# Optimization experiments

Hardware: AMD Instinct MI355X
Metric: run time of the kernel (lower is better)

## Reference

```python
import math
import jax, jax.numpy as jnp
import numpy as np

B, S, HID = 2, 1024, 1024
NH, HD = 16, 64
WIN = 4096
CACHE = 3072
EPS = 1e-5


def _clinear(xr, xi, Wr, Wi, br, bi):
    # complex linear: (xr + i xi)(Wr + i Wi)^T + (br + i bi)
    yr = xr @ Wr.T - xi @ Wi.T + br
    yi = xr @ Wi.T + xi @ Wr.T + bi
    return yr, yi


def _forward(hidden_re, hidden_im, K_cache_re, K_cache_im, V_cache_re, V_cache_im,
             gamma, beta_re, beta_im,
             q_Wr, q_Wi, q_br, q_bi, k_Wr, k_Wi, k_br, k_bi,
             v_Wr, v_Wi, v_br, v_bi, o_Wr, o_Wi, o_br, o_bi):
    batch, seq, _ = hidden_re.shape
    # --- complex LayerNorm: center complex mean, normalize by sqrt(E|x-mu|^2) ---
    mur = hidden_re.mean(-1, keepdims=True)
    mui = hidden_im.mean(-1, keepdims=True)
    cr = hidden_re - mur
    ci = hidden_im - mui
    inv = jax.lax.rsqrt((cr * cr + ci * ci).mean(-1, keepdims=True) + EPS)
    nr = cr * inv * gamma + beta_re
    ni = ci * inv * gamma + beta_im
    # --- projections ---
    Qr, Qi = _clinear(nr, ni, q_Wr, q_Wi, q_br, q_bi)
    Kr, Ki = _clinear(nr, ni, k_Wr, k_Wi, k_br, k_bi)
    Vr, Vi = _clinear(nr, ni, v_Wr, v_Wi, v_br, v_bi)
    Qr = Qr.reshape(batch, seq, NH, HD)
    Qi = Qi.reshape(batch, seq, NH, HD)
    Kr = Kr.reshape(batch, seq, NH, HD)
    Ki = Ki.reshape(batch, seq, NH, HD)
    Vr = Vr.reshape(batch, seq, NH, HD)
    Vi = Vi.reshape(batch, seq, NH, HD)
    # --- KV cache concat + window eviction (static shapes) ---
    cache_len = K_cache_re.shape[1]
    Kr = jnp.concatenate([K_cache_re, Kr], axis=1)
    Ki = jnp.concatenate([K_cache_im, Ki], axis=1)
    Vr = jnp.concatenate([V_cache_re, Vr], axis=1)
    Vi = jnp.concatenate([V_cache_im, Vi], axis=1)
    total_kv = Kr.shape[1]
    if total_kv > WIN:
        drop = total_kv - WIN
        Kr, Ki, Vr, Vi = Kr[:, drop:], Ki[:, drop:], Vr[:, drop:], Vi[:, drop:]
        cache_len = max(0, cache_len - drop)
        total_kv = WIN
    # --- Hermitian scores: Re(Q K^H) = Qr.Kr + Qi.Ki ---
    scale = 1.0 / math.sqrt(HD)
    scores = (jnp.einsum('bshd,bthd->bhst', Qr, Kr)
              + jnp.einsum('bshd,bthd->bhst', Qi, Ki)) * scale
    rows = jnp.arange(seq)[:, None]
    cols = jnp.arange(total_kv)[None, :]
    allowed = cols <= rows + cache_len  # causal within current chunk, full cache visible
    scores = jnp.where(allowed, scores, jnp.float32(-1e30))
    weights = jax.nn.softmax(scores, axis=-1)  # [B,NH,S,T]
    outr = jnp.einsum('bhst,bthd->bshd', weights, Vr).reshape(batch, seq, NH * HD)
    outi = jnp.einsum('bhst,bthd->bshd', weights, Vi).reshape(batch, seq, NH * HD)
    dr, di = _clinear(outr, outi, o_Wr, o_Wi, o_br, o_bi)
    out_re = hidden_re + dr
    out_im = hidden_im + di
    new_K_re, new_K_im = Kr[:, -WIN:], Ki[:, -WIN:]
    new_V_re, new_V_im = Vr[:, -WIN:], Vi[:, -WIN:]
    return out_re, out_im, new_K_re, new_K_im, new_V_re, new_V_im


def setup_inputs() -> dict:
    key = jax.random.key(0)
    ks = jax.random.split(key, 16)
    w = 0.02
    d = {
        'hidden_re': jax.random.normal(ks[0], (B, S, HID), jnp.float32),
        'hidden_im': jax.random.normal(ks[1], (B, S, HID), jnp.float32),
        'K_cache_re': jax.random.normal(ks[2], (B, CACHE, NH, HD), jnp.float32),
        'K_cache_im': jax.random.normal(ks[3], (B, CACHE, NH, HD), jnp.float32),
        'V_cache_re': jax.random.normal(ks[4], (B, CACHE, NH, HD), jnp.float32),
        'V_cache_im': jax.random.normal(ks[5], (B, CACHE, NH, HD), jnp.float32),
        'gamma': jnp.ones((HID,), jnp.float32),
        'beta_re': jnp.zeros((HID,), jnp.float32),
        'beta_im': jnp.zeros((HID,), jnp.float32),
    }
    for i, p in enumerate(['q', 'k', 'v', 'o']):
        d[p + '_Wr'] = jax.random.normal(ks[6 + 2 * i], (HID, HID), jnp.float32) * w
        d[p + '_Wi'] = jax.random.normal(ks[7 + 2 * i], (HID, HID), jnp.float32) * w
        d[p + '_br'] = jnp.zeros((HID,), jnp.float32)
        d[p + '_bi'] = jnp.zeros((HID,), jnp.float32)
    return d


def reference(hidden_re, hidden_im, K_cache_re, K_cache_im, V_cache_re, V_cache_im,
              gamma, beta_re, beta_im,
              q_Wr, q_Wi, q_br, q_bi, k_Wr, k_Wi, k_br, k_bi,
              v_Wr, v_Wi, v_br, v_bi, o_Wr, o_Wi, o_br, o_bi):
    return _forward(hidden_re, hidden_im, K_cache_re, K_cache_im, V_cache_re, V_cache_im,
                    gamma, beta_re, beta_im,
                    q_Wr, q_Wi, q_br, q_bi, k_Wr, k_Wi, k_br, k_bi,
                    v_Wr, v_Wi, v_br, v_bi, o_Wr, o_Wi, o_br, o_bi)
```

## Files before the change

kernel.cpp:

```cpp
#include <hip/hip_runtime.h>
#include <hip/hip_bf16.h>
#include <cstdint>
#include <cstddef>

typedef __bf16 bf16x8 __attribute__((ext_vector_type(8)));
typedef float  f32x4  __attribute__((ext_vector_type(4)));

__device__ __forceinline__ unsigned short f2bf(float f) {
  union { float f; unsigned u; } v; v.f = f;
  unsigned u = v.u;
  u += 0x7FFFu + ((u >> 16) & 1u);
  return (unsigned short)(u >> 16);
}

__device__ __forceinline__ unsigned short f2bf_cvt(float f) {
  __bf16 h = (__bf16)f;
  return __builtin_bit_cast(unsigned short, h);
}

struct alignas(16) US8 { unsigned short u[8]; };

__device__ __forceinline__ void g2lds16(const void* g, void* l) {
  __builtin_amdgcn_global_load_lds(
      (const __attribute__((address_space(1))) unsigned int*)g,
      (__attribute__((address_space(3))) unsigned int*)l, 16, 0, 0);
}

#define BB 2
#define SS 1024
#define HID 1024
#define NHH 16
#define HDD 64
#define TT 4096
#define CCH 3072
#define QSCALE (0.125f * 1.44269504088896f)

__global__ __launch_bounds__(256) void ln_kernel(
    const float* __restrict__ hre, const float* __restrict__ him,
    const float* __restrict__ gamma, const float* __restrict__ bre,
    const float* __restrict__ bim, unsigned short* __restrict__ Aln)
{
  int m = blockIdx.x;
  int tid = threadIdx.x;
  const float4 vr = ((const float4*)(hre + (size_t)m * HID))[tid];
  const float4 vi = ((const float4*)(him + (size_t)m * HID))[tid];
  float sr = vr.x + vr.y + vr.z + vr.w;
  float si = vi.x + vi.y + vi.z + vi.w;
  float sq = vr.x*vr.x + vr.y*vr.y + vr.z*vr.z + vr.w*vr.w
           + vi.x*vi.x + vi.y*vi.y + vi.z*vi.z + vi.w*vi.w;
  __shared__ float red[3][4];
  int lane = tid & 63, w = tid >> 6;
  for (int off = 32; off; off >>= 1) {
    sr += __shfl_down(sr, off, 64);
    si += __shfl_down(si, off, 64);
    sq += __shfl_down(sq, off, 64);
  }
  if (lane == 0) { red[0][w] = sr; red[1][w] = si; red[2][w] = sq; }
  __syncthreads();
  sr = red[0][0] + red[0][1] + red[0][2] + red[0][3];
  si = red[1][0] + red[1][1] + red[1][2] + red[1][3];
  sq = red[2][0] + red[2][1] + red[2][2] + red[2][3];
  float mur = sr * (1.f/1024.f), mui = si * (1.f/1024.f);
  float var = sq * (1.f/1024.f) - mur*mur - mui*mui;
  float inv = rsqrtf(var + 1e-5f);
  int k = tid * 4;
  float4 g  = ((const float4*)gamma)[tid];
  float4 br = ((const float4*)bre)[tid];
  float4 bi = ((const float4*)bim)[tid];
  ushort4 nr, ni;
  nr.x = f2bf((vr.x - mur) * inv * g.x + br.x);
  nr.y = f2bf((vr.y - mur) * inv * g.y + br.y);
  nr.z = f2bf((vr.z - mur) * inv * g.z + br.z);
  nr.w = f2bf((vr.w - mur) * inv * g.w + br.w);
  ni.x = f2bf((vi.x - mui) * inv * g.x + bi.x);
  ni.y = f2bf((vi.y - mui) * inv * g.y + bi.y);
  ni.z = f2bf((vi.z - mui) * inv * g.z + bi.z);
  ni.w = f2bf((vi.w - mui) * inv * g.w + bi.w);
  *(ushort4*)&Aln[(size_t)m * 2048 + k]        = nr;
  *(ushort4*)&Aln[(size_t)m * 2048 + 1024 + k] = ni;
}

__global__ __launch_bounds__(256) void wprep_kernel(
    const float* __restrict__ qWr, const float* __restrict__ qWi,
    const float* __restrict__ kWr, const float* __restrict__ kWi,
    const float* __restrict__ vWr, const float* __restrict__ vWi,
    const float* __restrict__ oWr, const float* __restrict__ oWi,
    unsigned short* __restrict__ Wc)
{
  int gid = blockIdx.x * 256 + threadIdx.x;
  int idx = gid * 8;
  int p   = idx >> 22;
  int rem = idx & 0x3FFFFF;
  int n   = rem >> 11;
  int k   = rem & 2047;
  const float* Wr; const float* Wi;
  switch (p) {
    case 0:  Wr = qWr; Wi = qWi; break;
    case 1:  Wr = kWr; Wi = kWi; break;
    case 2:  Wr = vWr; Wi = vWi; break;
    default: Wr = oWr; Wi = oWi; break;
  }
  const float* src; float sgn = 1.f;
  if (n < 1024) {
    if (k < 1024) src = Wr + (size_t)n * 1024 + k;
    else        { src = Wi + (size_t)n * 1024 + (k - 1024); sgn = -1.f; }
  } else {
    if (k < 1024) src = Wi + (size_t)(n - 1024) * 1024 + k;
    else          src = Wr + (size_t)(n - 1024) * 1024 + (k - 1024);
  }
  float4 a = ((const float4*)src)[0];
  float4 b = ((const float4*)src)[1];
  US8 o;
  o.u[0] = f2bf(a.x * sgn); o.u[1] = f2bf(a.y * sgn);
  o.u[2] = f2bf(a.z * sgn); o.u[3] = f2bf(a.w * sgn);
  o.u[4] = f2bf(b.x * sgn); o.u[5] = f2bf(b.y * sgn);
  o.u[6] = f2bf(b.z * sgn); o.u[7] = f2bf(b.w * sgn);
  *(US8*)&Wc[idx] = o;
}

__global__ __launch_bounds__(256) void bprep_kernel(
    const float* __restrict__ qbr, const float* __restrict__ qbi,
    const float* __restrict__ kbr, const float* __restrict__ kbi,
    const float* __restrict__ vbr, const float* __restrict__ vbi,
    const float* __restrict__ obr, const float* __restrict__ obi,
    float* __restrict__ bc)
{
  int idx = blockIdx.x * 256 + threadIdx.x;
  int p = idx >> 11, n = idx & 2047;
  const float* br; const float* bi;
  switch (p) {
    case 0:  br = qbr; bi = qbi; break;
    case 1:  br = kbr; bi = kbi; break;
    case 2:  br = vbr; bi = vbi; break;
    default: br = obr; bi = obi; break;
  }
  bc[idx] = (n < 1024) ? br[n] : bi[n - 1024];
}

__global__ __launch_bounds__(256) void gemm_qkv_kernel(
    const unsigned short* __restrict__ A, const unsigned short* __restrict__ Bm,
    const float* __restrict__ bias,
    unsigned short* __restrict__ Qp, unsigned short* __restrict__ Kp,
    float* __restrict__ out_Kre, float* __restrict__ out_Kim,
    float* __restrict__ out_Vre, float* __restrict__ out_Vim)
{
  __shared__ alignas(16) unsigned short As[128][32];
  __shared__ alignas(16) unsigned short Bs[128][32];
  const int K = 2048;
  int bm = blockIdx.y * 128;
  int bn = blockIdx.x * 128;
  int tid = threadIdx.x;
  int lane = tid & 63, w = tid >> 6;
  int wm = (w >> 1) * 64, wn = (w & 1) * 64;
  int l15 = lane & 15, q = lane >> 4;
  int lr = tid >> 2;
  int lc = (tid & 3) * 8;

  f32x4 acc[4][4] = {};

  for (int k0 = 0; k0 < K; k0 += 32) {
    g2lds16(&A [(size_t)(bm + lr)      * K + k0 + lc], (unsigned short*)As + 8*tid);
    g2lds16(&A [(size_t)(bm + lr + 64) * K + k0 + lc], (unsigned short*)As + 2048 + 8*tid);
    g2lds16(&Bm[(size_t)(bn + lr)      * K + k0 + lc], (unsigned short*)Bs + 8*tid);
    g2lds16(&Bm[(size_t)(bn + lr + 64) * K + k0 + lc], (unsigned short*)Bs + 2048 + 8*tid);
    __syncthreads();
    bf16x8 af[4], bfr[4];
#pragma unroll
    for (int i = 0; i < 4; i++) af[i]  = *(const bf16x8*)&As[wm + i*16 + l15][q*8];
#pragma unroll
    for (int i = 0; i < 4; i++) bfr[i] = *(const bf16x8*)&Bs[wn + i*16 + l15][q*8];
#pragma unroll
    for (int i = 0; i < 4; i++)
#pragma unroll
      for (int j = 0; j < 4; j++)
        acc[i][j] = __builtin_amdgcn_mfma_f32_16x16x32_bf16(af[i], bfr[j], acc[i][j], 0, 0, 0);
    __syncthreads();
  }

  const int sec = bn >> 11;
#pragma unroll
  for (int i = 0; i < 4; i++)
#pragma unroll
    for (int j = 0; j < 4; j++) {
      int n = bn + wn + j*16 + l15;
      float bv = bias[n];
      int col = n & 2047;
      int re = (col < 1024) ? 1 : 0;
      int h = (col & 1023) >> 6, d = col & 63;
      int d2 = re ? d : 64 + d;
#pragma unroll
      for (int r = 0; r < 4; r++) {
        int m = bm + wm + i*16 + q*4 + r;
        float val = acc[i][j][r] + bv;
        int b = m >> 10, s = m & 1023;
        int bh = b*16 + h;
        if (sec == 0) {
          Qp[((size_t)bh*1024 + s)*128 + d2] = f2bf(val * QSCALE);
        } else if (sec == 1) {
          int t = CCH + s;
          Kp[((size_t)bh*4096 + t)*128 + d2] = f2bf(val);
          float* dst = re ? out_Kre : out_Kim;
          dst[(((size_t)b*4096 + t)*16 + h)*64 + d] = val;
        } else {
          int t = CCH + s;
          float* dst = re ? out_Vre : out_Vim;
          dst[(((size_t)b*4096 + t)*16 + h)*64 + d] = val;
        }
      }
    }
}

__global__ __launch_bounds__(256) void gemm_oproj_kernel(
    const unsigned short* __restrict__ A, const unsigned short* __restrict__ Bm,
    const float* __restrict__ bias, const float* __restrict__ hre,
    const float* __restrict__ him, float* __restrict__ out)
{
  __shared__ alignas(16) unsigned short As[128][32];
  __shared__ alignas(16) unsigned short Bs[128][32];
  int bm = blockIdx.y * 128;
  int bn = blockIdx.x * 128;
  int tid = threadIdx.x;
  int lane = tid & 63, w = tid >> 6;
  int wm = (w >> 1) * 64, wn = (w & 1) * 64;
  int l15 = lane & 15, q = lane >> 4;
  int lr = tid >> 2;
  int lc = (tid & 3) * 8;
  const int K = 2048;

  f32x4 acc[4][4] = {};

  for (int k0 = 0; k0 < K; k0 += 32) {
    g2lds16(&A [(size_t)(bm + lr)      * K + k0 + lc], (unsigned short*)As + 8*tid);
    g2lds16(&A [(size_t)(bm + lr + 64) * K + k0 + lc], (unsigned short*)As + 2048 + 8*tid);
    g2lds16(&Bm[(size_t)(bn + lr)      * K + k0 + lc], (unsigned short*)Bs + 8*tid);
    g2lds16(&Bm[(size_t)(bn + lr + 64) * K + k0 + lc], (unsigned short*)Bs + 2048 + 8*tid);
    __syncthreads();
    bf16x8 af[4], bfr[4];
#pragma unroll
    for (int i = 0; i < 4; i++) af[i]  = *(const bf16x8*)&As[wm + i*16 + l15][q*8];
#pragma unroll
    for (int i = 0; i < 4; i++) bfr[i] = *(const bf16x8*)&Bs[wn + i*16 + l15][q*8];
#pragma unroll
    for (int i = 0; i < 4; i++)
#pragma unroll
      for (int j = 0; j < 4; j++)
        acc[i][j] = __builtin_amdgcn_mfma_f32_16x16x32_bf16(af[i], bfr[j], acc[i][j], 0, 0, 0);
    __syncthreads();
  }

#pragma unroll
  for (int i = 0; i < 4; i++)
#pragma unroll
    for (int j = 0; j < 4; j++) {
      int n = bn + wn + j*16 + l15;
      float bv = bias[n];
#pragma unroll
      for (int r = 0; r < 4; r++) {
        int m = bm + wm + i*16 + q*4 + r;
        float val = acc[i][j][r] + bv;
        if (n < 1024) out[(size_t)m * 1024 + n] = val + hre[(size_t)m * 1024 + n];
        else out[2097152 + (size_t)m * 1024 + (n - 1024)] = val + him[(size_t)m * 1024 + (n - 1024)];
      }
    }
}

__global__ __launch_bounds__(256) void pack_kcache_kernel(
    const float* __restrict__ c_re, const float* __restrict__ c_im,
    unsigned short* __restrict__ Kp,
    float* __restrict__ out_re, float* __restrict__ out_im)
{
  int bh = blockIdx.y;
  int idx = (blockIdx.x * 256 + threadIdx.x) * 4;
  int d2 = idx & 127;
  int t  = idx >> 7;
  int b = bh >> 4, h = bh & 15;
  int d = d2 & 63;
  bool im = d2 >= 64;
  const float* src = im ? c_im : c_re;
  float4 v = *(const float4*)&src[(((size_t)b * CCH + t) * 16 + h) * 64 + d];
  ushort4 o;
  o.x = f2bf(v.x); o.y = f2bf(v.y); o.z = f2bf(v.z); o.w = f2bf(v.w);
  *(ushort4*)&Kp[((size_t)bh * 4096 + t) * 128 + d2] = o;
  float* dst = im ? out_im : out_re;
  *(float4*)&dst[(((size_t)b * 4096 + t) * 16 + h) * 64 + d] = v;
}

__global__ __launch_bounds__(256) void pack_vt_fused_kernel(
    const float* __restrict__ Vc_re, const float* __restrict__ Vc_im,
    float* __restrict__ out_Vre, float* __restrict__ out_Vim,
    unsigned short* __restrict__ Vt)
{
  __shared__ float Ts[64][136];
  const int ty = blockIdx.x & 63;
  const int bh = blockIdx.x >> 6;
  const int b = bh >> 4, h = bh & 15;
  const int t0 = ty * 64;
  const int tid = threadIdx.x;
#pragma unroll
  for (int rr = 0; rr < 8; rr++) {
    int j = rr * 256 + tid;
    int t_loc = j >> 5, c = j & 31;
    int d2 = c * 4;
    int t = t0 + t_loc;
    int d = (d2 < 64) ? d2 : d2 - 64;
    float4 v;
    if (t < CCH) {
      const float* src = (d2 < 64) ? Vc_re : Vc_im;
      v = *(const float4*)&src[(((size_t)b * CCH + t) * 16 + h) * 64 + d];
      float* dst = (d2 < 64) ? out_Vre : out_Vim;
      *(float4*)&dst[(((size_t)b * 4096 + t) * 16 + h) * 64 + d] = v;
    } else {
      const float* src = (d2 < 64) ? out_Vre : out_Vim;
      v = *(const float4*)&src[(((size_t)b * 4096 + t) * 16 + h) * 64 + d];
    }
    *(float4*)&Ts[t_loc][d2] = v;
  }
  __syncthreads();
  const int d2 = tid >> 1, half = tid & 1;
  unsigned short tmp[32];
#pragma unroll
  for (int i = 0; i < 32; i++) tmp[i] = f2bf(Ts[half*32 + i][d2]);
  size_t dst = (size_t)bh * 128 * 4096 + (size_t)d2 * 4096 + t0 + half*32;
#pragma unroll
  for (int kq = 0; kq < 4; kq++)
    *(US8*)&Vt[dst + kq*8] = *(US8*)&tmp[kq*8];
}

__global__ __launch_bounds__(256) void attn_kernel(
    const unsigned short* __restrict__ Qp, const unsigned short* __restrict__ Kp,
    const unsigned short* __restrict__ Vt, float* __restrict__ Opart,
    float* __restrict__ Lpart)
{
  const int bh   = blockIdx.x;
  const int sblk = blockIdx.y;
  const int tpar = blockIdx.z;
  const int s0 = sblk * 128;
  const int tid = threadIdx.x;
  const int lane = tid & 63, w = tid >> 6;
  const int l15 = lane & 15, q = lane >> 4;

  __shared__ alignas(16) unsigned short Ks[2][32][128];
  __shared__ alignas(16) unsigned short Vs[2][128][32];
  __shared__ alignas(16) unsigned short Ps[4][32][40];

  bf16x8 qf[2][4];
#pragma unroll
  for (int mi = 0; mi < 2; mi++) {
    const size_t qb = ((size_t)bh * 1024 + s0 + w*32 + mi*16 + l15) * 128;
#pragma unroll
    for (int kc = 0; kc < 4; kc++)
      qf[mi][kc] = *(const bf16x8*)&Qp[qb + kc*32 + q*8];
  }

  f32x4 oacc[2][8] = {};
  float lsum[2][4] = {};

  const size_t kpb = (size_t)bh * 4096 * 128;
  const size_t vtb = (size_t)bh * 128 * 4096;
  const int n_tiles = 4*sblk + 100;
  const int n_safe  = n_tiles - 4;

  auto issue = [&](int buf, int t0) {
#pragma unroll
    for (int kk = 0; kk < 2; kk++) {
      int j = (w*2 + kk)*64 + lane;
      int r = j >> 4, p = j & 15, c = p ^ (r & 7);
      g2lds16(&Kp[kpb + (size_t)(t0 + r) * 128 + c*8],
              (unsigned short*)&Ks[buf][0][0] + (size_t)j * 8);
    }
#pragma unroll
    for (int kk = 0; kk < 2; kk++) {
      int j = (w*2 + kk)*64 + lane;
      int r = j >> 2, p = j & 3, c = p ^ (r & 3);
      g2lds16(&Vt[vtb + (size_t)r * 4096 + t0 + c*8],
              (unsigned short*)&Vs[buf][0][0] + (size_t)j * 8);
    }
  };

  int buf = 0;
  issue(0, tpar * 32);

  for (int it = tpar; it < n_tiles; it += 3) {
    __syncthreads();
    if (it + 3 < n_tiles) issue(buf ^ 1, (it + 3) * 32);

    f32x4 sacc[2][2] = {};
    __builtin_amdgcn_s_setprio(1);
#pragma unroll
    for (int kc = 0; kc < 4; kc++) {
      bf16x8 kf[2];
#pragma unroll
      for (int nc = 0; nc < 2; nc++)
        kf[nc] = *(const bf16x8*)&Ks[buf][nc*16 + l15][((kc*4 + q) ^ (l15 & 7)) * 8];
#pragma unroll
      for (int mi = 0; mi < 2; mi++)
#pragma unroll
        for (int nc = 0; nc < 2; nc++)
          sacc[mi][nc] = __builtin_amdgcn_mfma_f32_16x16x32_bf16(qf[mi][kc], kf[nc], sacc[mi][nc], 0, 0, 0);
    }
    __builtin_amdgcn_s_setprio(0);

    const bool safe = (it < n_safe);
    const int t0 = it << 5;
#pragma unroll
    for (int mi = 0; mi < 2; mi++)
#pragma unroll
      for (int r = 0; r < 4; r++) {
        const int rr = mi*16 + q*4 + r;
        const int rel = s0 + w*32 + rr + CCH - t0;
        float ls = 0.f;
#pragma unroll
        for (int nc = 0; nc < 2; nc++) {
          float p;
          asm("v_exp_f32 %0, %1" : "=v"(p) : "v"(sacc[mi][nc][r]));
          if (!safe && (nc*16 + l15 > rel)) p = 0.f;
          ls += p;
          Ps[w][rr][nc*16 + l15] = f2bf_cvt(p);
        }
        lsum[mi][r] += ls;
      }

    bf16x8 pf[2];
#pragma unroll
    for (int mi = 0; mi < 2; mi++)
      pf[mi] = *(const bf16x8*)&Ps[w][mi*16 + l15][q*8];
    __builtin_amdgcn_s_setprio(1);
#pragma unroll
    for (int dc = 0; dc < 8; dc++) {
      int d2 = dc*16 + l15;
      bf16x8 vfr = *(const bf16x8*)&Vs[buf][d2][(q ^ (d2 & 3)) * 8];
#pragma unroll
      for (int mi = 0; mi < 2; mi++)
        oacc[mi][dc] = __builtin_amdgcn_mfma_f32_16x16x32_bf16(pf[mi], vfr, oacc[mi][dc], 0, 0, 0);
    }
    __builtin_amdgcn_s_setprio(0);
    buf ^= 1;
  }

  const size_t pb = ((size_t)tpar * 32 + bh) * 1024 + s0 + w*32;
#pragma unroll
  for (int mi = 0; mi < 2; mi++)
#pragma unroll
    for (int r = 0; r < 4; r++) {
      float l = lsum[mi][r];
      l += __shfl_xor(l, 1, 64);
      l += __shfl_xor(l, 2, 64);
      l += __shfl_xor(l, 4, 64);
      l += __shfl_xor(l, 8, 64);
      if (l15 == 0) Lpart[pb + mi*16 + q*4 + r] = l;
    }
#pragma unroll
  for (int mi = 0; mi < 2; mi++)
#pragma unroll
    for (int dc = 0; dc < 8; dc++)
#pragma unroll
      for (int r = 0; r < 4; r++)
        Opart[(pb + mi*16 + q*4 + r) * 128 + dc*16 + l15] = oacc[mi][dc][r];
}

__global__ __launch_bounds__(256) void attn_combine_kernel(
    const float* __restrict__ Opart, const float* __restrict__ Lpart,
    unsigned short* __restrict__ Ao)
{
  const size_t TS = 4194304ull;
  int gid = blockIdx.x * 256 + threadIdx.x;
  int idx = gid * 8;
  int m = idx >> 11, n0 = idx & 2047;
  int b = m >> 10, s = m & 1023;
  int h, d2_0;
  if (n0 < 1024) { h = n0 >> 6; d2_0 = n0 & 63; }
  else { h = (n0 - 1024) >> 6; d2_0 = 64 + ((n0 - 1024) & 63); }
  int bh = b*16 + h;
  size_t ob = ((size_t)bh * 1024 + s) * 128 + d2_0;
  float l0 = Lpart[(size_t)bh * 1024 + s];
  float l1 = Lpart[32768 + (size_t)bh * 1024 + s];
  float l2 = Lpart[65536 + (size_t)bh * 1024 + s];
  float inv = 1.f / (l0 + l1 + l2);
  float4 x0 = *(const float4*)&Opart[ob];
  float4 x1 = *(const float4*)&Opart[ob + 4];
  float4 y0 = *(const float4*)&Opart[ob + TS];
  float4 y1 = *(const float4*)&Opart[ob + TS + 4];
  float4 z0 = *(const float4*)&Opart[ob + 2*TS];
  float4 z1 = *(const float4*)&Opart[ob + 2*TS + 4];
  US8 o;
  o.u[0] = f2bf((x0.x + y0.x + z0.x) * inv); o.u[1] = f2bf((x0.y + y0.y + z0.y) * inv);
  o.u[2] = f2bf((x0.z + y0.z + z0.z) * inv); o.u[3] = f2bf((x0.w + y0.w + z0.w) * inv);
  o.u[4] = f2bf((x1.x + y1.x + z1.x) * inv); o.u[5] = f2bf((x1.y + y1.y + z1.y) * inv);
  o.u[6] = f2bf((x1.z + y1.z + z1.z) * inv); o.u[7] = f2bf((x1.w + y1.w + z1.w) * inv);
  *(US8*)&Ao[idx] = o;
}

extern "C" void kernel_launch(void* const* d_in, const int* in_sizes, int n_in,
                              void* d_out, int out_size, void* d_ws, size_t ws_size,
                              hipStream_t stream)
{
  (void)in_sizes; (void)n_in; (void)out_size; (void)ws_size;
  const float* hre = (const float*)d_in[0];
  const float* him = (const float*)d_in[1];
  const float* Kcr = (const float*)d_in[2];
  const float* Kci = (const float*)d_in[3];
  const float* Vcr = (const float*)d_in[4];
  const float* Vci = (const float*)d_in[5];
  const float* gamma = (const float*)d_in[6];
  const float* bre = (const float*)d_in[7];
  const float* bim = (const float*)d_in[8];
  const float* qWr = (const float*)d_in[9];
  const float* qWi = (const float*)d_in[10];
  const float* qbr = (const float*)d_in[11];
  const float* qbi = (const float*)d_in[12];
  const float* kWr = (const float*)d_in[13];
  const float* kWi = (const float*)d_in[14];
  const float* kbr = (const float*)d_in[15];
  const float* kbi = (const float*)d_in[16];
  const float* vWr = (const float*)d_in[17];
  const float* vWi = (const float*)d_in[18];
  const float* vbr = (const float*)d_in[19];
  const float* vbi = (const float*)d_in[20];
  const float* oWr = (const float*)d_in[21];
  const float* oWi = (const float*)d_in[22];
  const float* obr = (const float*)d_in[23];
  const float* obi = (const float*)d_in[24];
  float* out = (float*)d_out;

  char* ws = (char*)d_ws;
  size_t off = 0;
  auto carve = [&](size_t bytes) {
    char* p = ws + off;
    off += (bytes + 255) & ~(size_t)255;
    return p;
  };
  unsigned short* Aln  = (unsigned short*)carve(2048ull * 2048 * 2);
  unsigned short* Wc   = (unsigned short*)carve(4ull * 2048 * 2048 * 2);
  float*          bc   = (float*)carve(4ull * 2048 * 4);
  unsigned short* Qp   = (unsigned short*)carve(4194304ull * 2);
  unsigned short* Kp   = (unsigned short*)carve(16777216ull * 2);
  unsigned short* Vt   = (unsigned short*)carve(16777216ull * 2);
  float*          Opart= (float*)carve(3ull * 32 * 1024 * 128 * 4);
  float*          Lpart= (float*)carve(3ull * 32 * 1024 * 4);

  unsigned short* Ao = Aln;

  float* out_Kre = out + 4194304;
  float* out_Kim = out + 4194304 + 8388608;
  float* out_Vre = out + 4194304 + 2 * 8388608;
  float* out_Vim = out + 4194304 + 3 * 8388608;

  hipLaunchKernelGGL(ln_kernel, dim3(2048), dim3(256), 0, stream,
                     hre, him, gamma, bre, bim, Aln);
  hipLaunchKernelGGL(wprep_kernel, dim3(8192), dim3(256), 0, stream,
                     qWr, qWi, kWr, kWi, vWr, vWi, oWr, oWi, Wc);
  hipLaunchKernelGGL(bprep_kernel, dim3(32), dim3(256), 0, stream,
                     qbr, qbi, kbr, kbi, vbr, vbi, obr, obi, bc);
  hipLaunchKernelGGL(gemm_qkv_kernel, dim3(48, 16), dim3(256), 0, stream,
                     Aln, Wc, bc, Qp, Kp, out_Kre, out_Kim, out_Vre, out_Vim);
  hipLaunchKernelGGL(pack_kcache_kernel, dim3(384, 32), dim3(256), 0, stream,
                     Kcr, Kci, Kp, out_Kre, out_Kim);
  hipLaunchKernelGGL(pack_vt_fused_kernel, dim3(2048), dim3(256), 0, stream,
                     Vcr, Vci, out_Vre, out_Vim, Vt);
  hipLaunchKernelGGL(attn_kernel, dim3(32, 8, 3), dim3(256), 0, stream,
                     Qp, Kp, Vt, Opart, Lpart);
  hipLaunchKernelGGL(attn_combine_kernel, dim3(2048), dim3(256), 0, stream,
                     Opart, Lpart, Ao);
  hipLaunchKernelGGL(gemm_oproj_kernel, dim3(16, 16), dim3(256), 0, stream,
                     Ao, Wc + 3ull * 2048 * 2048, bc + 3 * 2048, hre, him, out);
}
```

Measured before the change: 598.6 us.

## Triple-buffer GEMM LDS staging and swizzle LDS layouts to cut bank conflicts

The QKV and output-projection GEMMs now use a three-stage LDS ring buffer. Global-to-LDS loads for tile t+2 are issued while tile t is computed, with explicit vmcnt waits and a single barrier per iteration instead of two syncthreads. The LDS column layout is XOR-swizzled by row for the GEMM tiles and the attention V tile, to reduce bank conflicts on the 16-byte fragment reads. This triples GEMM shared memory per block, which may lower occupancy, and relies on the hand-written waitcnt counts being correct.

```diff
diff --git a/kernel.cpp b/kernel.cpp
--- a/kernel.cpp
+++ b/kernel.cpp
@@ -144,9 +144,10 @@
     float* __restrict__ out_Kre, float* __restrict__ out_Kim,
     float* __restrict__ out_Vre, float* __restrict__ out_Vim)
 {
-  __shared__ alignas(16) unsigned short As[128][32];
-  __shared__ alignas(16) unsigned short Bs[128][32];
+  __shared__ alignas(16) unsigned short As[3][128][32];
+  __shared__ alignas(16) unsigned short Bs[3][128][32];
   const int K = 2048;
+  const int NT = K / 32;
   int bm = blockIdx.y * 128;
   int bn = blockIdx.x * 128;
   int tid = threadIdx.x;
@@ -154,27 +155,48 @@
   int wm = (w >> 1) * 64, wn = (w & 1) * 64;
   int l15 = lane & 15, q = lane >> 4;
   int lr = tid >> 2;
-  int lc = (tid & 3) * 8;
+  int lcs = ((tid & 3) ^ ((tid >> 3) & 3)) * 8;
+
+  const unsigned short* A0 = A  + (size_t)(bm + lr)      * K + lcs;
+  const unsigned short* A1 = A  + (size_t)(bm + lr + 64) * K + lcs;
+  const unsigned short* B0 = Bm + (size_t)(bn + lr)      * K + lcs;
+  const unsigned short* B1 = Bm + (size_t)(bn + lr + 64) * K + lcs;
+  const int rsw = ((l15 >> 1) & 3);
 
   f32x4 acc[4][4] = {};
 
-  for (int k0 = 0; k0 < K; k0 += 32) {
-    g2lds16(&A [(size_t)(bm + lr)      * K + k0 + lc], (unsigned short*)As + 8*tid);
-    g2lds16(&A [(size_t)(bm + lr + 64) * K + k0 + lc], (unsigned short*)As + 2048 + 8*tid);
-    g2lds16(&Bm[(size_t)(bn + lr)      * K + k0 + lc], (unsigned short*)Bs + 8*tid);
-    g2lds16(&Bm[(size_t)(bn + lr + 64) * K + k0 + lc], (unsigned short*)Bs + 2048 + 8*tid);
-    __syncthreads();
+  auto stage = [&](int b, int t) {
+    int k0 = t * 32;
+    g2lds16(A0 + k0, (unsigned short*)As[b] + 8*tid);
+    g2lds16(A1 + k0, (unsigned short*)As[b] + 2048 + 8*tid);
+    g2lds16(B0 + k0, (unsigned short*)Bs[b] + 8*tid);
+    g2lds16(B1 + k0, (unsigned short*)Bs[b] + 2048 + 8*tid);
+  };
+
+  stage(0, 0);
+  stage(1, 1);
+
+  int bc_ = 0, bp_ = 2;
+  for (int t = 0; t < NT; ++t) {
+    if (t + 1 < NT) asm volatile("s_waitcnt vmcnt(4)" ::: "memory");
+    else            asm volatile("s_waitcnt vmcnt(0)" ::: "memory");
+    __builtin_amdgcn_s_barrier();
+    __builtin_amdgcn_sched_barrier(0);
+    if (t + 2 < NT) stage(bp_, t + 2);
+
     bf16x8 af[4], bfr[4];
 #pragma unroll
-    for (int i = 0; i < 4; i++) af[i]  = *(const bf16x8*)&As[wm + i*16 + l15][q*8];
-#pragma unroll
-    for (int i = 0; i < 4; i++) bfr[i] = *(const bf16x8*)&Bs[wn + i*16 + l15][q*8];
+    for (int i = 0; i < 4; i++) af[i]  = *(const bf16x8*)&As[bc_][wm + i*16 + l15][(q ^ rsw) * 8];
+#pragma unroll
+    for (int i = 0; i < 4; i++) bfr[i] = *(const bf16x8*)&Bs[bc_][wn + i*16 + l15][(q ^ rsw) * 8];
 #pragma unroll
     for (int i = 0; i < 4; i++)
 #pragma unroll
       for (int j = 0; j < 4; j++)
         acc[i][j] = __builtin_amdgcn_mfma_f32_16x16x32_bf16(af[i], bfr[j], acc[i][j], 0, 0, 0);
-    __syncthreads();
+
+    bc_ = (bc_ == 2) ? 0 : bc_ + 1;
+    bp_ = (bp_ == 2) ? 0 : bp_ + 1;
   }
 
   const int sec = bn >> 11;
@@ -215,8 +237,10 @@
     const float* __restrict__ bias, const float* __restrict__ hre,
     const float* __restrict__ him, float* __restrict__ out)
 {
-  __shared__ alignas(16) unsigned short As[128][32];
-  __shared__ alignas(16) unsigned short Bs[128][32];
+  __shared__ alignas(16) unsigned short As[3][128][32];
+  __shared__ alignas(16) unsigned short Bs[3][128][32];
+  const int K = 2048;
+  const int NT = K / 32;
   int bm = blockIdx.y * 128;
   int bn = blockIdx.x * 128;
   int tid = threadIdx.x;
@@ -224,28 +248,48 @@
   int wm = (w >> 1) * 64, wn = (w & 1) * 64;
   int l15 = lane & 15, q = lane >> 4;
   int lr = tid >> 2;
-  int lc = (tid & 3) * 8;
-  const int K = 2048;
+  int lcs = ((tid & 3) ^ ((tid >> 3) & 3)) * 8;
+
+  const unsigned short* A0 = A  + (size_t)(bm + lr)      * K + lcs;
+  const unsigned short* A1 = A  + (size_t)(bm + lr + 64) * K + lcs;
+  const unsigned short* B0 = Bm + (size_t)(bn + lr)      * K + lcs;
+  const unsigned short* B1 = Bm + (size_t)(bn + lr + 64) * K + lcs;
+  const int rsw = ((l15 >> 1) & 3);
 
   f32x4 acc[4][4] = {};
 
-  for (int k0 = 0; k0 < K; k0 += 32) {
-    g2lds16(&A [(size_t)(bm + lr)      * K + k0 + lc], (unsigned short*)As + 8*tid);
-    g2lds16(&A [(size_t)(bm + lr + 64) * K + k0 + lc], (unsigned short*)As + 2048 + 8*tid);
-    g2lds16(&Bm[(size_t)(bn + lr)      * K + k0 + lc], (unsigned short*)Bs + 8*tid);
-    g2lds16(&Bm[(size_t)(bn + lr + 64) * K + k0 + lc], (unsigned short*)Bs + 2048 + 8*tid);
-    __syncthreads();
+  auto stage = [&](int b, int t) {
+    int k0 = t * 32;
+    g2lds16(A0 + k0, (unsigned short*)As[b] + 8*tid);
+    g2lds16(A1 + k0, (unsigned short*)As[b] + 2048 + 8*tid);
+    g2lds16(B0 + k0, (unsigned short*)Bs[b] + 8*tid);
+    g2lds16(B1 + k0, (unsigned short*)Bs[b] + 2048 + 8*tid);
+  };
+
+  stage(0, 0);
+  stage(1, 1);
+
+  int bc_ = 0, bp_ = 2;
+  for (int t = 0; t < NT; ++t) {
+    if (t + 1 < NT) asm volatile("s_waitcnt vmcnt(4)" ::: "memory");
+    else            asm volatile("s_waitcnt vmcnt(0)" ::: "memory");
+    __builtin_amdgcn_s_barrier();
+    __builtin_amdgcn_sched_barrier(0);
+    if (t + 2 < NT) stage(bp_, t + 2);
+
     bf16x8 af[4], bfr[4];
 #pragma unroll
-    for (int i = 0; i < 4; i++) af[i]  = *(const bf16x8*)&As[wm + i*16 + l15][q*8];
-#pragma unroll
-    for (int i = 0; i < 4; i++) bfr[i] = *(const bf16x8*)&Bs[wn + i*16 + l15][q*8];
+    for (int i = 0; i < 4; i++) af[i]  = *(const bf16x8*)&As[bc_][wm + i*16 + l15][(q ^ rsw) * 8];
+#pragma unroll
+    for (int i = 0; i < 4; i++) bfr[i] = *(const bf16x8*)&Bs[bc_][wn + i*16 + l15][(q ^ rsw) * 8];
 #pragma unroll
     for (int i = 0; i < 4; i++)
 #pragma unroll
       for (int j = 0; j < 4; j++)
         acc[i][j] = __builtin_amdgcn_mfma_f32_16x16x32_bf16(af[i], bfr[j], acc[i][j], 0, 0, 0);
-    __syncthreads();
+
+    bc_ = (bc_ == 2) ? 0 : bc_ + 1;
+    bp_ = (bp_ == 2) ? 0 : bp_ + 1;
   }
 
 #pragma unroll
@@ -371,7 +415,7 @@
 #pragma unroll
     for (int kk = 0; kk < 2; kk++) {
       int j = (w*2 + kk)*64 + lane;
-      int r = j >> 2, p = j & 3, c = p ^ (r & 3);
+      int r = j >> 2, p = j & 3, c = p ^ ((r >> 1) & 3);
       g2lds16(&Vt[vtb + (size_t)r * 4096 + t0 + c*8],
               (unsigned short*)&Vs[buf][0][0] + (size_t)j * 8);
     }
@@ -428,7 +472,7 @@
 #pragma unroll
     for (int dc = 0; dc < 8; dc++) {
       int d2 = dc*16 + l15;
-      bf16x8 vfr = *(const bf16x8*)&Vs[buf][d2][(q ^ (d2 & 3)) * 8];
+      bf16x8 vfr = *(const bf16x8*)&Vs[buf][d2][(q ^ ((d2 >> 1) & 3)) * 8];
 #pragma unroll
       for (int mi = 0; mi < 2; mi++)
         oacc[mi][dc] = __builtin_amdgcn_mfma_f32_16x16x32_bf16(pf[mi], vfr, oacc[mi][dc], 0, 0, 0);
```

New measurement: 572.1 us. 1.05x faster.
